# Kernel tuning notes

Hardware: AMD Instinct MI355X
Metric: run time of the kernel (lower is better)

The kernel has to match this reference:

```python
import jax, jax.numpy as jnp
import numpy as np

B, T, C, HID, K, H = 8, 1024, 512, 2048, 31, 4  # batch, time, in_chans, hidden_chans, kernel, wshare


def setup_inputs() -> dict:
    key = jax.random.key(0)
    ks = jax.random.split(key, 8)
    n = lambda k_, sh, sc: jax.random.normal(k_, sh, dtype=jnp.float32) * sc
    return {
        "x": n(ks[0], (B, T, C), 1.0),
        "Wl": n(ks[1], (H * K, C), 0.05),      # linear_weight.weight
        "bl": n(ks[2], (H * K,), 0.01),          # linear_weight.bias
        "bias": n(ks[3], (C,), 0.02),            # self.bias
        "Wc": n(ks[4], (HID, C, K), 0.01),       # pointwise_conv1.weight (O,I,K)
        "bc": n(ks[5], (HID,), 0.01),            # pointwise_conv1.bias
        "W2": n(ks[6], (C, HID), 0.01),          # w_2.weight
        "b2": n(ks[7], (C,), 0.01),              # w_2.bias
    }


def reference(x, Wl, bl, bias, Wc, bc, W2, b2):
    Bq, Tq, Cq = x.shape
    d = Cq // H  # channels per weight-share head
    # dynamic conv logits: (B,T,H,K)
    logits = (x @ Wl.T + bl).reshape(Bq, Tq, H, K)
    # banded positions: output t attends to t + j - (K-1)//2
    offs = jnp.arange(K) - (K - 1) // 2
    pos = jnp.arange(Tq)[:, None] + offs[None, :]          # (T,K)
    valid = (pos >= 0) & (pos < Tq)
    logits = jnp.where(valid[None, :, None, :], logits, -jnp.inf)
    w = jax.nn.softmax(logits, axis=-1)                     # softmax over window (matches banded softmax over T)
    # gather windowed inputs: (B,T,K,H,d)
    xg = x.reshape(Bq, Tq, H, d)[:, jnp.clip(pos, 0, Tq - 1)]
    y = jnp.einsum('bthk,btkhd->bthd', w, xg).reshape(Bq, Tq, Cq)
    # (B,C,T) + bias
    y = y.transpose(0, 2, 1) + bias[None, :, None]
    # pointwise_conv1: Conv1d(C->HID, kernel K, padding 0) -> T' = T-K+1
    z = jax.lax.conv_general_dilated(y, Wc, (1,), 'VALID',
                                     dimension_numbers=('NCH', 'OIH', 'NCH'))
    z = z + bc[None, :, None]
    z = jax.nn.selu(z.transpose(0, 2, 1))                   # (B,T',HID)
    return z @ W2.T + b2                                    # (B,T',C)
```

## Files before the change

### kernel.cpp

```cpp
#include <hip/hip_runtime.h>
#include <hip/hip_bf16.h>

typedef __attribute__((ext_vector_type(8))) short short8;
typedef __attribute__((ext_vector_type(4))) float f32x4;

#define NB 8
#define NT 1024
#define NC 512
#define NHID 2048
#define NK 31
#define NH 4
#define NTP 994
#define MROWS (NB * NTP)
#define TG 4

__device__ __forceinline__ void gload_lds16(const void* g, void* l) {
  __builtin_amdgcn_global_load_lds(
      (const __attribute__((address_space(1))) void*)g,
      (__attribute__((address_space(3))) void*)l, 16, 0, 0);
}

__global__ __launch_bounds__(256) void prep_wc(const float* __restrict__ Wc,
                                               __hip_bfloat16* __restrict__ Wt) {
  const int blk = blockIdx.x;
  const int cb = blk & 7;
  const int o0 = (blk >> 3) << 3;
  const int c0 = cb << 6;
  const int obig = o0 >> 8;
  const int orb = o0 & 255;
  __shared__ float lds[8 * 64 * NK];
  for (int ol = 0; ol < 8; ++ol) {
    const float* src = Wc + ((size_t)(o0 + ol) * NC + c0) * NK;
    for (int i = threadIdx.x; i < 64 * NK; i += 256) lds[ol * (64 * NK) + i] = src[i];
  }
  __syncthreads();
  for (int i = threadIdx.x; i < NK * 8 * 64; i += 256) {
    const int k = i >> 9;
    const int rem = i & 511;
    const int ol = rem >> 6;
    const int ci = rem & 63;
    Wt[((size_t)((obig * 8 + cb) * NK + k) << 14) + ((orb + ol) << 6) + (ci ^ (ol << 3))] =
        __float2bfloat16(lds[ol * (64 * NK) + ci * NK + k]);
  }
}

__global__ __launch_bounds__(256) void prep_w2(const float* __restrict__ W2,
                                               __hip_bfloat16* __restrict__ W2t) {
  const int i = blockIdx.x * 256 + threadIdx.x;
  if (i < 32 * 512 * 64) {
    const int oi = i & 63;
    const int c = (i >> 6) & 511;
    const int kb = i >> 15;
    const size_t dst = ((size_t)(((c >> 7) * 32 + kb) * 128 + (c & 127)) << 6) +
                       (oi ^ ((c & 7) << 3));
    W2t[dst] = __float2bfloat16(W2[(size_t)c * NHID + (kb << 6) + oi]);
  }
}

__global__ __launch_bounds__(256) void dynconv(const float* __restrict__ x,
                                               const float* __restrict__ Wl,
                                               const float* __restrict__ bl,
                                               const float* __restrict__ bias,
                                               __hip_bfloat16* __restrict__ Y) {
  const int t0 = blockIdx.x * TG;
  const int b = blockIdx.y;
  const int tid = threadIdx.x, lane = tid & 63, w = tid >> 6;
  __shared__ float xt[TG][NC];
  __shared__ float lg[TG][NH * NK];
  __shared__ float wsm[TG][NH][NK];

  for (int i = tid; i < TG * NC; i += 256) {
    const int tg = i >> 9, c = i & 511;
    xt[tg][c] = x[((size_t)b * NT + t0 + tg) * NC + c];
  }
  __syncthreads();

  for (int i = 0; i < 31; ++i) {
    const int id = (i << 2) | w;
    const float* wrow = Wl + (size_t)id * NC + (lane << 3);
    float wv[8];
#pragma unroll
    for (int u = 0; u < 8; ++u) wv[u] = wrow[u];
    const float blv = bl[id];
#pragma unroll
    for (int tg = 0; tg < TG; ++tg) {
      float s = 0.f;
#pragma unroll
      for (int u = 0; u < 8; ++u) s += xt[tg][(lane << 3) + u] * wv[u];
#pragma unroll
      for (int off = 32; off; off >>= 1) s += __shfl_xor(s, off);
      if (lane == 0) lg[tg][id] = s + blv;
    }
  }
  __syncthreads();

  if (tid < TG * NH) {
    const int tg = tid >> 2, h = tid & 3;
    const int t = t0 + tg;
    int jlo = 15 - t; if (jlo < 0) jlo = 0;
    int jhi = 1038 - t; if (jhi > 30) jhi = 30;
    float mx = -1e30f;
    for (int j = jlo; j <= jhi; ++j) mx = fmaxf(mx, lg[tg][h * NK + j]);
    float ssum = 0.f;
    for (int j = 0; j < NK; ++j) {
      const float e = (j >= jlo && j <= jhi) ? __expf(lg[tg][h * NK + j] - mx) : 0.f;
      wsm[tg][h][j] = e;
      ssum += e;
    }
    const float inv = 1.f / ssum;
    for (int j = 0; j < NK; ++j) wsm[tg][h][j] *= inv;
  }
  __syncthreads();

  const int c = tid << 1;
  const int h = c >> 7;
  const float2* x2 = (const float2*)x;
  const float bias0 = bias[c], bias1 = bias[c + 1];
#pragma unroll
  for (int tg = 0; tg < TG; ++tg) {
    const int t = t0 + tg;
    float a0 = 0.f, a1 = 0.f;
#pragma unroll
    for (int j = 0; j < NK; ++j) {
      int pos = t + j - 15;
      pos = pos < 0 ? 0 : (pos > NT - 1 ? NT - 1 : pos);
      const float wgt = wsm[tg][h][j];
      const float2 v = x2[(((size_t)b * NT + pos) << 8) + tid];
      a0 += wgt * v.x;
      a1 += wgt * v.y;
    }
    const int cs = (c & ~63) | ((c & 63) ^ ((t & 7) << 3));
    __hip_bfloat162 hv;
    hv.x = __float2bfloat16(a0 + bias0);
    hv.y = __float2bfloat16(a1 + bias1);
    *(__hip_bfloat162*)(Y + ((size_t)b * NT + t) * NC + cs) = hv;
  }
}

__global__ __launch_bounds__(512, 2) void conv_gemm(const __hip_bfloat16* __restrict__ Y,
                                                    const __hip_bfloat16* __restrict__ Wt,
                                                    const float* __restrict__ bc,
                                                    __hip_bfloat16* __restrict__ Z) {
  const int o0 = blockIdx.x << 8;
  const int t0 = blockIdx.y << 8;
  const int b = blockIdx.z;
  __shared__ __align__(16) __hip_bfloat16 Ys[288 * 64];
  __shared__ __align__(16) __hip_bfloat16 Bs[2][256 * 64];
  const int tid = threadIdx.x;
  const int lane = tid & 63, wid = tid >> 6;
  const int wr = wid >> 2, wcid = wid & 3;
  const int obig = o0 >> 8;

  f32x4 acc[8][4] = {};

  auto stageY = [&](int cb_) {
    const int c0 = cb_ << 6;
#pragma unroll
    for (int p = 0; p < 5; ++p) {
      const int i = (p << 9) + tid;
      if (i < 2304) {
        int grow = t0 + (i >> 3);
        if (grow > NT - 1) grow = NT - 1;
        gload_lds16(Y + (((size_t)b * NT + grow) << 9) + c0 + ((i & 7) << 3),
                    &Ys[i << 3]);
      }
    }
  };
  auto stageB = [&](int bufi, int s_) {
    const __hip_bfloat16* wb = Wt + (((size_t)(obig * 248 + s_)) << 14);
#pragma unroll
    for (int p = 0; p < 4; ++p) {
      const int i = (p << 9) + tid;
      gload_lds16(wb + (i << 3), &Bs[bufi][i << 3]);
    }
  };

  stageY(0);
  stageB(0, 0);

  int buf = 0;
  for (int cb = 0; cb < 8; ++cb) {
    for (int k = 0; k < NK; ++k) {
      const int s = cb * 31 + k;
      if (s < 247) {
        stageB(buf ^ 1, s + 1);
        asm volatile("s_waitcnt vmcnt(4)" ::: "memory");
      } else {
        asm volatile("s_waitcnt vmcnt(0)" ::: "memory");
      }
      __builtin_amdgcn_sched_barrier(0);
      __builtin_amdgcn_s_barrier();
      __builtin_amdgcn_sched_barrier(0);

      __builtin_amdgcn_s_setprio(1);
#pragma unroll
      for (int kk = 0; kk < 2; ++kk) {
        const int ko = (kk << 5) + ((lane >> 4) << 3);
        short8 av[8], bv[4];
#pragma unroll
        for (int m = 0; m < 8; ++m) {
          const int r2 = (wr << 7) + (m << 4) + (lane & 15) + k;
          av[m] = *(const short8*)&Ys[(r2 << 6) + (ko ^ ((r2 & 7) << 3))];
        }
#pragma unroll
        for (int n = 0; n < 4; ++n) {
          const int br = (wcid << 6) + (n << 4) + (lane & 15);
          bv[n] = *(const short8*)&Bs[buf][(br << 6) + (ko ^ ((br & 7) << 3))];
        }
#pragma unroll
        for (int m = 0; m < 8; ++m)
#pragma unroll
          for (int n = 0; n < 4; ++n)
            acc[m][n] = __builtin_amdgcn_mfma_f32_16x16x32_bf16(av[m], bv[n], acc[m][n], 0, 0, 0);
      }
      __builtin_amdgcn_s_setprio(0);

      __builtin_amdgcn_sched_barrier(0);
      __builtin_amdgcn_s_barrier();
      __builtin_amdgcn_sched_barrier(0);
      buf ^= 1;
    }
    if (cb < 7) stageY(cb + 1);
  }

  const float kS = 1.0507009873554805f;
  const float kAS = 1.7580993408473766f;
#pragma unroll
  for (int n = 0; n < 4; ++n) {
    const int col = o0 + (wcid << 6) + (n << 4) + (lane & 15);
    const float bcv = bc[col];
#pragma unroll
    for (int m = 0; m < 8; ++m) {
      const int rbase = (wr << 7) + (m << 4) + ((lane >> 4) << 2);
#pragma unroll
      for (int r = 0; r < 4; ++r) {
        const int tp = t0 + rbase + r;
        if (tp < NTP) {
          const float v = acc[m][n][r] + bcv;
          const float s = v > 0.f ? kS * v : kAS * (__expf(v) - 1.f);
          const size_t grow = (size_t)b * NTP + tp;
          const int cs = (col & ~63) | ((col & 63) ^ (((int)(grow & 7)) << 3));
          Z[grow * NHID + cs] = __float2bfloat16(s);
        }
      }
    }
  }
}

__global__ __launch_bounds__(256) void out_gemm(const __hip_bfloat16* __restrict__ Zm,
                                                const __hip_bfloat16* __restrict__ W2t,
                                                const float* __restrict__ b2,
                                                float* __restrict__ Out) {
  const int n0 = blockIdx.x << 7;
  const int m0 = blockIdx.y << 7;
  __shared__ __align__(16) __hip_bfloat16 As[128 * 64];
  __shared__ __align__(16) __hip_bfloat16 Bs[128 * 64];
  const int tid = threadIdx.x;
  const int lane = tid & 63, wid = tid >> 6;
  const int wr = wid >> 1, wc = wid & 1;

  f32x4 acc[4][4] = {};

  for (int kb = 0; kb < 32; ++kb) {
#pragma unroll
    for (int p = 0; p < 4; ++p) {
      const int i = (p << 8) + tid;
      int row = m0 + (i >> 3);
      if (row > MROWS - 1) row = MROWS - 1;
      gload_lds16(Zm + ((size_t)row << 11) + (kb << 6) + ((i & 7) << 3), &As[i << 3]);
    }
    const __hip_bfloat16* wb = W2t + ((size_t)((n0 >> 7) * 32 + kb) << 13);
#pragma unroll
    for (int p = 0; p < 4; ++p) {
      const int i = (p << 8) + tid;
      gload_lds16(wb + (i << 3), &Bs[i << 3]);
    }
    __syncthreads();
#pragma unroll
    for (int kk = 0; kk < 2; ++kk) {
      const int ko = (kk << 5) + ((lane >> 4) << 3);
      short8 av[4], bv[4];
#pragma unroll
      for (int m = 0; m < 4; ++m) {
        const int r = (wr << 6) + (m << 4) + (lane & 15);
        av[m] = *(const short8*)&As[(r << 6) + (ko ^ ((r & 7) << 3))];
      }
#pragma unroll
      for (int n = 0; n < 4; ++n) {
        const int br = (wc << 6) + (n << 4) + (lane & 15);
        bv[n] = *(const short8*)&Bs[(br << 6) + (ko ^ ((br & 7) << 3))];
      }
#pragma unroll
      for (int m = 0; m < 4; ++m)
#pragma unroll
        for (int n = 0; n < 4; ++n)
          acc[m][n] = __builtin_amdgcn_mfma_f32_16x16x32_bf16(av[m], bv[n], acc[m][n], 0, 0, 0);
    }
    __syncthreads();
  }

#pragma unroll
  for (int n = 0; n < 4; ++n) {
    const int col = n0 + (wc << 6) + (n << 4) + (lane & 15);
    const float b2v = b2[col];
#pragma unroll
    for (int m = 0; m < 4; ++m) {
      const int rbase = m0 + (wr << 6) + (m << 4) + ((lane >> 4) << 2);
#pragma unroll
      for (int r = 0; r < 4; ++r) {
        const int row = rbase + r;
        if (row < MROWS) Out[(size_t)row * NC + col] = acc[m][n][r] + b2v;
      }
    }
  }
}

extern "C" void kernel_launch(void* const* d_in, const int* in_sizes, int n_in,
                              void* d_out, int out_size, void* d_ws, size_t ws_size,
                              hipStream_t stream) {
  const float* x = (const float*)d_in[0];
  const float* Wl = (const float*)d_in[1];
  const float* bl = (const float*)d_in[2];
  const float* bias = (const float*)d_in[3];
  const float* Wc = (const float*)d_in[4];
  const float* bc = (const float*)d_in[5];
  const float* W2 = (const float*)d_in[6];
  const float* b2 = (const float*)d_in[7];
  float* out = (float*)d_out;

  char* ws = (char*)d_ws;
  __hip_bfloat16* Wt = (__hip_bfloat16*)(ws);
  __hip_bfloat16* Y = (__hip_bfloat16*)(ws + 65011712);
  __hip_bfloat16* W2t = (__hip_bfloat16*)(ws + 73400320);
  __hip_bfloat16* Z = (__hip_bfloat16*)(ws + 75497472);

  hipLaunchKernelGGL(prep_wc, dim3(2048), dim3(256), 0, stream, Wc, Wt);
  hipLaunchKernelGGL(prep_w2, dim3(4096), dim3(256), 0, stream, W2, W2t);
  hipLaunchKernelGGL(dynconv, dim3(NT / TG, NB), dim3(256), 0, stream, x, Wl, bl, bias, Y);
  hipLaunchKernelGGL(conv_gemm, dim3(NHID / 256, 4, NB), dim3(512), 0, stream, Y, Wt, bc, Z);
  hipLaunchKernelGGL(out_gemm, dim3(NC / 128, (MROWS + 127) / 128), dim3(256), 0, stream,
                     Z, W2t, b2, out);
}
```

Baseline: 707.5 us.

## Stream conv weights directly to registers, stage epilogue in LDS, double-buffer out GEMM

The conv GEMM no longer stages the weight tile through double-buffered LDS with barriers. Each lane loads its B fragments straight from global memory (the weight swizzle is removed to match), and the per-step barriers are dropped. The epilogue writes SELU results to an LDS tile and then stores them to Z as coalesced 16-byte rows, and the output GEMM gains double-buffered LDS staging. The dynconv kernel vectorizes its loads to float4 and caches x in registers. Loading weights straight from global removes LDS traffic and barriers but exposes global latency inside the MFMA loop, and the 135 KB LDS pool likely limits the conv kernel to one block per CU.

```diff
diff --git a/kernel.cpp b/kernel.cpp
--- a/kernel.cpp
+++ b/kernel.cpp
@@ -2,6 +2,7 @@
 #include <hip/hip_bf16.h>
 
 typedef __attribute__((ext_vector_type(8))) short short8;
+typedef __attribute__((ext_vector_type(4))) short short4v;
 typedef __attribute__((ext_vector_type(4))) float f32x4;
 
 #define NB 8
@@ -39,7 +40,7 @@
     const int rem = i & 511;
     const int ol = rem >> 6;
     const int ci = rem & 63;
-    Wt[((size_t)((obig * 8 + cb) * NK + k) << 14) + ((orb + ol) << 6) + (ci ^ (ol << 3))] =
+    Wt[((size_t)((obig * 8 + cb) * NK + k) << 14) + ((orb + ol) << 6) + ci] =
         __float2bfloat16(lds[ol * (64 * NK) + ci * NK + k]);
   }
 }
@@ -69,11 +70,19 @@
   __shared__ float lg[TG][NH * NK];
   __shared__ float wsm[TG][NH][NK];
 
-  for (int i = tid; i < TG * NC; i += 256) {
-    const int tg = i >> 9, c = i & 511;
-    xt[tg][c] = x[((size_t)b * NT + t0 + tg) * NC + c];
-  }
-  __syncthreads();
+  {
+    const float4* xsrc = (const float4*)(x + ((size_t)b * NT + t0) * NC);
+    float4* xdst = (float4*)xt;
+#pragma unroll
+    for (int i = 0; i < 2; ++i) xdst[(i << 8) + tid] = xsrc[(i << 8) + tid];
+  }
+  __syncthreads();
+
+  float xv[TG][8];
+#pragma unroll
+  for (int tg = 0; tg < TG; ++tg)
+#pragma unroll
+    for (int u = 0; u < 8; ++u) xv[tg][u] = xt[tg][(lane << 3) + u];
 
   for (int i = 0; i < 31; ++i) {
     const int id = (i << 2) | w;
@@ -86,7 +95,7 @@
     for (int tg = 0; tg < TG; ++tg) {
       float s = 0.f;
 #pragma unroll
-      for (int u = 0; u < 8; ++u) s += xt[tg][(lane << 3) + u] * wv[u];
+      for (int u = 0; u < 8; ++u) s += xv[tg][u] * wv[u];
 #pragma unroll
       for (int off = 32; off; off >>= 1) s += __shfl_xor(s, off);
       if (lane == 0) lg[tg][id] = s + blv;
@@ -112,28 +121,30 @@
   }
   __syncthreads();
 
-  const int c = tid << 1;
-  const int h = c >> 7;
-  const float2* x2 = (const float2*)x;
-  const float bias0 = bias[c], bias1 = bias[c + 1];
-#pragma unroll
-  for (int tg = 0; tg < TG; ++tg) {
+  const int grp = tid >> 7;
+  const int ct = tid & 127;
+  const int c4 = ct << 2;
+  const int h = c4 >> 7;
+  const float4* x4 = (const float4*)x;
+  const float4 b4 = ((const float4*)bias)[ct];
+  for (int tg = grp; tg < TG; tg += 2) {
     const int t = t0 + tg;
-    float a0 = 0.f, a1 = 0.f;
+    float a0 = 0.f, a1 = 0.f, a2 = 0.f, a3 = 0.f;
 #pragma unroll
     for (int j = 0; j < NK; ++j) {
       int pos = t + j - 15;
       pos = pos < 0 ? 0 : (pos > NT - 1 ? NT - 1 : pos);
       const float wgt = wsm[tg][h][j];
-      const float2 v = x2[(((size_t)b * NT + pos) << 8) + tid];
-      a0 += wgt * v.x;
-      a1 += wgt * v.y;
-    }
-    const int cs = (c & ~63) | ((c & 63) ^ ((t & 7) << 3));
-    __hip_bfloat162 hv;
-    hv.x = __float2bfloat16(a0 + bias0);
-    hv.y = __float2bfloat16(a1 + bias1);
-    *(__hip_bfloat162*)(Y + ((size_t)b * NT + t) * NC + cs) = hv;
+      const float4 v = x4[(((size_t)b * NT + pos) << 7) + ct];
+      a0 += wgt * v.x; a1 += wgt * v.y; a2 += wgt * v.z; a3 += wgt * v.w;
+    }
+    const int cs = (c4 & ~63) | ((c4 & 63) ^ ((t & 7) << 3));
+    union { short4v s4; __hip_bfloat16 hh[4]; } u;
+    u.hh[0] = __float2bfloat16(a0 + b4.x);
+    u.hh[1] = __float2bfloat16(a1 + b4.y);
+    u.hh[2] = __float2bfloat16(a2 + b4.z);
+    u.hh[3] = __float2bfloat16(a3 + b4.w);
+    *(short4v*)(Y + ((size_t)b * NT + t) * NC + cs) = u.s4;
   }
 }
 
@@ -144,12 +155,14 @@
   const int o0 = blockIdx.x << 8;
   const int t0 = blockIdx.y << 8;
   const int b = blockIdx.z;
-  __shared__ __align__(16) __hip_bfloat16 Ys[288 * 64];
-  __shared__ __align__(16) __hip_bfloat16 Bs[2][256 * 64];
+  __shared__ __align__(16) char pool[135168];
+  __hip_bfloat16* Ys = (__hip_bfloat16*)pool;
   const int tid = threadIdx.x;
   const int lane = tid & 63, wid = tid >> 6;
   const int wr = wid >> 2, wcid = wid & 3;
   const int obig = o0 >> 8;
+  const int l15 = lane & 15;
+  const int kob = (lane >> 4) << 3;
 
   f32x4 acc[8][4] = {};
 
@@ -166,83 +179,80 @@
       }
     }
   };
-  auto stageB = [&](int bufi, int s_) {
-    const __hip_bfloat16* wb = Wt + (((size_t)(obig * 248 + s_)) << 14);
-#pragma unroll
-    for (int p = 0; p < 4; ++p) {
-      const int i = (p << 9) + tid;
-      gload_lds16(wb + (i << 3), &Bs[bufi][i << 3]);
-    }
-  };
+
+  const __hip_bfloat16* wlane =
+      Wt + (((size_t)(obig * 248)) << 14) + (((wcid << 6) + l15) << 6) + kob;
 
   stageY(0);
-  stageB(0, 0);
-
-  int buf = 0;
+  __syncthreads();
+
   for (int cb = 0; cb < 8; ++cb) {
     for (int k = 0; k < NK; ++k) {
       const int s = cb * 31 + k;
-      if (s < 247) {
-        stageB(buf ^ 1, s + 1);
-        asm volatile("s_waitcnt vmcnt(4)" ::: "memory");
-      } else {
-        asm volatile("s_waitcnt vmcnt(0)" ::: "memory");
-      }
-      __builtin_amdgcn_sched_barrier(0);
-      __builtin_amdgcn_s_barrier();
-      __builtin_amdgcn_sched_barrier(0);
-
+      const __hip_bfloat16* wt = wlane + ((size_t)s << 14);
+      short8 bv[2][4];
+#pragma unroll
+      for (int n = 0; n < 4; ++n) {
+        bv[0][n] = *(const short8*)(wt + (n << 10));
+        bv[1][n] = *(const short8*)(wt + (n << 10) + 32);
+      }
+      const int keyv = ((l15 + k) & 7) << 3;
+      const int ako0 = kob ^ keyv;
+      const int ako1 = (32 | kob) ^ keyv;
+      const int arow = ((wr << 7) + l15 + k) << 6;
+      short8 av[2][8];
+#pragma unroll
+      for (int m = 0; m < 8; ++m) {
+        av[0][m] = *(const short8*)&Ys[arow + (m << 10) + ako0];
+        av[1][m] = *(const short8*)&Ys[arow + (m << 10) + ako1];
+      }
       __builtin_amdgcn_s_setprio(1);
 #pragma unroll
-      for (int kk = 0; kk < 2; ++kk) {
-        const int ko = (kk << 5) + ((lane >> 4) << 3);
-        short8 av[8], bv[4];
-#pragma unroll
-        for (int m = 0; m < 8; ++m) {
-          const int r2 = (wr << 7) + (m << 4) + (lane & 15) + k;
-          av[m] = *(const short8*)&Ys[(r2 << 6) + (ko ^ ((r2 & 7) << 3))];
-        }
-#pragma unroll
-        for (int n = 0; n < 4; ++n) {
-          const int br = (wcid << 6) + (n << 4) + (lane & 15);
-          bv[n] = *(const short8*)&Bs[buf][(br << 6) + (ko ^ ((br & 7) << 3))];
-        }
+      for (int kk = 0; kk < 2; ++kk)
 #pragma unroll
         for (int m = 0; m < 8; ++m)
 #pragma unroll
           for (int n = 0; n < 4; ++n)
-            acc[m][n] = __builtin_amdgcn_mfma_f32_16x16x32_bf16(av[m], bv[n], acc[m][n], 0, 0, 0);
-      }
+            acc[m][n] = __builtin_amdgcn_mfma_f32_16x16x32_bf16(av[kk][m], bv[kk][n],
+                                                                acc[m][n], 0, 0, 0);
       __builtin_amdgcn_s_setprio(0);
-
-      __builtin_amdgcn_sched_barrier(0);
-      __builtin_amdgcn_s_barrier();
-      __builtin_amdgcn_sched_barrier(0);
-      buf ^= 1;
-    }
-    if (cb < 7) stageY(cb + 1);
-  }
-
+    }
+    if (cb < 7) {
+      __syncthreads();
+      stageY(cb + 1);
+      __syncthreads();
+    }
+  }
+
+  __syncthreads();
+  __hip_bfloat16* zt = (__hip_bfloat16*)pool;
   const float kS = 1.0507009873554805f;
   const float kAS = 1.7580993408473766f;
 #pragma unroll
   for (int n = 0; n < 4; ++n) {
-    const int col = o0 + (wcid << 6) + (n << 4) + (lane & 15);
-    const float bcv = bc[col];
+    const int col = (wcid << 6) + (n << 4) + l15;
+    const float bcv = bc[o0 + col];
 #pragma unroll
     for (int m = 0; m < 8; ++m) {
-      const int rbase = (wr << 7) + (m << 4) + ((lane >> 4) << 2);
+      const int rb = (wr << 7) + (m << 4) + ((lane >> 4) << 2);
 #pragma unroll
       for (int r = 0; r < 4; ++r) {
-        const int tp = t0 + rbase + r;
-        if (tp < NTP) {
-          const float v = acc[m][n][r] + bcv;
-          const float s = v > 0.f ? kS * v : kAS * (__expf(v) - 1.f);
-          const size_t grow = (size_t)b * NTP + tp;
-          const int cs = (col & ~63) | ((col & 63) ^ (((int)(grow & 7)) << 3));
-          Z[grow * NHID + cs] = __float2bfloat16(s);
-        }
-      }
+        const float v = acc[m][n][r] + bcv;
+        const float sv = v > 0.f ? kS * v : kAS * (__expf(v) - 1.f);
+        zt[(rb + r) * 264 + col] = __float2bfloat16(sv);
+      }
+    }
+  }
+  __syncthreads();
+  for (int j = tid; j < 8192; j += 512) {
+    const int row = j >> 5;
+    const int c8 = (j & 31) << 3;
+    const int tp = t0 + row;
+    if (tp < NTP) {
+      const size_t grow = (size_t)b * NTP + tp;
+      const int key = ((int)grow & 7) << 3;
+      const int cs = (c8 & ~63) | ((c8 & 63) ^ key);
+      *(short8*)(Z + grow * NHID + o0 + cs) = *(const short8*)&zt[row * 264 + c8];
     }
   }
 }
@@ -253,29 +263,36 @@
                                                 float* __restrict__ Out) {
   const int n0 = blockIdx.x << 7;
   const int m0 = blockIdx.y << 7;
-  __shared__ __align__(16) __hip_bfloat16 As[128 * 64];
-  __shared__ __align__(16) __hip_bfloat16 Bs[128 * 64];
+  __shared__ __align__(16) __hip_bfloat16 As[2][128 * 64];
+  __shared__ __align__(16) __hip_bfloat16 Bs[2][128 * 64];
   const int tid = threadIdx.x;
   const int lane = tid & 63, wid = tid >> 6;
   const int wr = wid >> 1, wc = wid & 1;
 
-  f32x4 acc[4][4] = {};
-
-  for (int kb = 0; kb < 32; ++kb) {
+  auto stage = [&](int bufi, int kb_) {
 #pragma unroll
     for (int p = 0; p < 4; ++p) {
       const int i = (p << 8) + tid;
       int row = m0 + (i >> 3);
       if (row > MROWS - 1) row = MROWS - 1;
-      gload_lds16(Zm + ((size_t)row << 11) + (kb << 6) + ((i & 7) << 3), &As[i << 3]);
-    }
-    const __hip_bfloat16* wb = W2t + ((size_t)((n0 >> 7) * 32 + kb) << 13);
+      gload_lds16(Zm + ((size_t)row << 11) + (kb_ << 6) + ((i & 7) << 3),
+                  &As[bufi][i << 3]);
+    }
+    const __hip_bfloat16* wb = W2t + ((size_t)((n0 >> 7) * 32 + kb_) << 13);
 #pragma unroll
     for (int p = 0; p < 4; ++p) {
       const int i = (p << 8) + tid;
-      gload_lds16(wb + (i << 3), &Bs[i << 3]);
-    }
+      gload_lds16(wb + (i << 3), &Bs[bufi][i << 3]);
+    }
+  };
+
+  f32x4 acc[4][4] = {};
+  stage(0, 0);
+
+  for (int kb = 0; kb < 32; ++kb) {
+    const int buf = kb & 1;
     __syncthreads();
+    if (kb < 31) stage(buf ^ 1, kb + 1);
 #pragma unroll
     for (int kk = 0; kk < 2; ++kk) {
       const int ko = (kk << 5) + ((lane >> 4) << 3);
@@ -283,12 +300,12 @@
 #pragma unroll
       for (int m = 0; m < 4; ++m) {
         const int r = (wr << 6) + (m << 4) + (lane & 15);
-        av[m] = *(const short8*)&As[(r << 6) + (ko ^ ((r & 7) << 3))];
+        av[m] = *(const short8*)&As[buf][(r << 6) + (ko ^ ((r & 7) << 3))];
       }
 #pragma unroll
       for (int n = 0; n < 4; ++n) {
         const int br = (wc << 6) + (n << 4) + (lane & 15);
-        bv[n] = *(const short8*)&Bs[(br << 6) + (ko ^ ((br & 7) << 3))];
+        bv[n] = *(const short8*)&Bs[buf][(br << 6) + (ko ^ ((br & 7) << 3))];
       }
 #pragma unroll
       for (int m = 0; m < 4; ++m)
@@ -296,7 +313,6 @@
         for (int n = 0; n < 4; ++n)
           acc[m][n] = __builtin_amdgcn_mfma_f32_16x16x32_bf16(av[m], bv[n], acc[m][n], 0, 0, 0);
     }
-    __syncthreads();
   }
 
 #pragma unroll
```

Measured after the change: 700.2 us. No clear change (-1.0%).
